# Kernel optimization log

Hardware: AMD Instinct MI355X
Metric: run time of the kernel (lower is better)

The kernel has to match this reference:

```python
import jax, jax.numpy as jnp
import numpy as np

N_STATE = 128      # HiPPO state size (hardcoded N=128 in module)
SEQ = 8192         # sequence length
D_HEAD = 16        # d_model=128 // n_head=8, used only for score scaling
OUT_DIM = 1000     # hardcoded self.out_dim
STEP = 1e-3        # step_size


def _legs_matrices(N):
    # HiPPO-LegS: A[n,k] = -sqrt(2n+1)sqrt(2k+1) (n>k), -(n+1) (n==k), 0 else; B[n]=sqrt(2n+1)
    n = np.arange(N, dtype=np.float64)
    pre = np.sqrt(2.0 * n + 1.0)
    A = -np.tril(pre[:, None] * pre[None, :], -1) - np.diag(n + 1.0)
    B = pre.copy()
    return A, B


def setup_inputs() -> dict:
    key = jax.random.key(0)
    kq, kk, kv, kw = jax.random.split(key, 4)
    A_np, B_np = _legs_matrices(N_STATE)
    A = jnp.asarray(A_np, jnp.float32)
    B = jnp.asarray(B_np, jnp.float32)
    # ZOH discretization (GBT_alpha=2.0 > 1 in repo => zero-order hold)
    GA = jax.scipy.linalg.expm(STEP * A)                       # (N, N)
    GB = jnp.linalg.solve(A, (GA - jnp.eye(N_STATE)) @ B)      # (N,)
    # xavier-uniform proj kernel (128 -> 1000), zero bias
    lim = float(np.sqrt(6.0 / (N_STATE + OUT_DIM)))
    Wp = jax.random.uniform(kw, (N_STATE, OUT_DIM), jnp.float32, -lim, lim)
    bp = jnp.zeros((OUT_DIM,), jnp.float32)
    return {
        "query": jax.random.normal(kq, (SEQ, 1), jnp.float32),
        "key": jax.random.normal(kk, (SEQ, 1), jnp.float32),
        "value": jax.random.normal(kv, (SEQ, 1), jnp.float32),
        "GA": GA,
        "GB": GB,
        "Wp": Wp,
        "bp": bp,
    }


def _hippo_scan(GA, GB, fs):
    # fs: (3, S) scalar input sequences; carry c: (3, N)
    def step(c, ft):
        c = c @ GA.T + ft[:, None] * GB[None, :]
        return c, c
    c0 = jnp.zeros((fs.shape[0], GA.shape[0]), GA.dtype)
    _, cs = jax.lax.scan(step, c0, fs.T)   # cs: (S, 3, N)
    return cs


def reference(query, key, value, GA, GB, Wp, bp):
    fs = jnp.stack([query[:, 0], key[:, 0], value[:, 0]])  # (3, S)
    cs = _hippo_scan(GA, GB, fs)                            # (S, 3, N)
    q, k, v = cs[:, 0, :], cs[:, 1, :], cs[:, 2, :]         # (S, N) each
    score = (q @ k.T) / jnp.sqrt(jnp.asarray(D_HEAD, q.dtype))  # (S, S)
    attn = jax.nn.softmax(score, axis=-1)
    context = attn @ v                                      # (S, N)
    out = context @ Wp + bp                                 # (S, OUT_DIM)
    return out, attn
```

## Files before the change

kernel.cpp:

```cpp
#include <hip/hip_runtime.h>

static constexpr int N  = 128;
static constexpr int S  = 8192;
static constexpr int L  = 128;
static constexpr int NC = 64;
static constexpr int OD = 1000;
static constexpr int KSPLIT = 16;
#define SCL 0.25f

typedef unsigned short u16;
typedef __attribute__((ext_vector_type(4))) unsigned short us4;
typedef __attribute__((ext_vector_type(8))) unsigned short us8;
typedef __attribute__((ext_vector_type(8))) short bf16x8;
typedef __attribute__((ext_vector_type(4))) float f32x4;

__device__ __forceinline__ u16 f2bf(float x){
  unsigned u = __float_as_uint(x);
  u += 0x7FFFu + ((u >> 16) & 1u);
  return (u16)(u >> 16);
}
__device__ __forceinline__ float bf2f(u16 h){
  return __uint_as_float(((unsigned)h) << 16);
}

__global__ void k_copyT(const float* __restrict__ GA, float* __restrict__ QT1){
  int idx = blockIdx.x*256 + threadIdx.x;
  int m = idx >> 7, n = idx & 127;
  QT1[idx] = GA[n*N + m];
}

__global__ __launch_bounds__(256) void k_powmm(float* QT, int mlev){
  int i = blockIdx.z + 1;
  const float* Am = QT + (size_t)mlev*(N*N);
  const float* Ai = QT + (size_t)i*(N*N);
  float* C = QT + (size_t)(mlev+i)*(N*N);
  __shared__ __align__(16) float As[16][68];
  __shared__ __align__(16) float Bs[16][68];
  int bm = blockIdx.y, bn = blockIdx.x;
  int tx = threadIdx.x, ty = threadIdx.y;
  int tid = ty*16 + tx;
  float acc[4][4] = {};
  for (int kt = 0; kt < N; kt += 16){
    int row = tid >> 2, kc = (tid & 3) << 2;
    float4 av = *(const float4*)(Am + (size_t)(bm*64+row)*N + kt + kc);
    As[kc+0][row]=av.x; As[kc+1][row]=av.y; As[kc+2][row]=av.z; As[kc+3][row]=av.w;
    int bk = tid >> 4, c0 = (tid & 15) << 2;
    *(float4*)&Bs[bk][c0] = *(const float4*)(Ai + (size_t)(kt+bk)*N + bn*64 + c0);
    __syncthreads();
#pragma unroll
    for (int kk = 0; kk < 16; ++kk){
      float4 a = *(const float4*)&As[kk][ty*4];
      float4 b = *(const float4*)&Bs[kk][tx*4];
      float aa[4]={a.x,a.y,a.z,a.w}, bb[4]={b.x,b.y,b.z,b.w};
#pragma unroll
      for (int ii=0; ii<4; ++ii)
#pragma unroll
        for (int jj=0; jj<4; ++jj) acc[ii][jj] += aa[ii]*bb[jj];
    }
    __syncthreads();
  }
#pragma unroll
  for (int ii=0; ii<4; ++ii){
    float4 vst = make_float4(acc[ii][0],acc[ii][1],acc[ii][2],acc[ii][3]);
    *(float4*)(C + (size_t)(bm*64+ty*4+ii)*N + bn*64 + tx*4) = vst;
  }
}

__global__ void k_g(const float* __restrict__ QT, const float* __restrict__ GB,
                    float* __restrict__ g){
  int kb = blockIdx.x;
  int n = threadIdx.x;
  if (kb == 0){ g[n] = GB[n]; return; }
  const float* Qk = QT + (size_t)kb*(N*N);
  float acc = 0.0f;
  for (int m = 0; m < N; ++m) acc += Qk[m*N + n]*GB[m];
  g[kb*N + n] = acc;
}

__global__ __launch_bounds__(256) void k_fill_local(const float* __restrict__ fq,
                             const float* __restrict__ fk, const float* __restrict__ fv,
                             const float* __restrict__ g, float* __restrict__ cs){
  int tile = blockIdx.x;
  int s = blockIdx.y, j = blockIdx.z;
  const float* f = (s==0)? fq : (s==1)? fk : fv;
  __shared__ float flp[256];
  __shared__ __align__(16) float Bs[16][68];
  int tx = threadIdx.x, ty = threadIdx.y;
  int tid = ty*16 + tx;
  flp[tid] = (tid < 128) ? 0.0f : f[j*L + tid - 128];
  int ti = tile >> 1, tj = tile & 1;
  float acc[4][4] = {};
  int kmax = (ti == 0) ? 64 : 128;
  for (int kt = 0; kt < kmax; kt += 16){
    int bk = tid >> 4, c0 = (tid & 15) << 2;
    *(float4*)&Bs[bk][c0] = *(const float4*)(g + (size_t)(kt+bk)*N + tj*64 + c0);
    __syncthreads();
#pragma unroll
    for (int kk = 0; kk < 16; ++kk){
      float4 b = *(const float4*)&Bs[kk][tx*4];
      int base = 128 + ti*64 + ty*4 - kt - kk;
      float aa[4] = {flp[base], flp[base+1], flp[base+2], flp[base+3]};
      float bb[4] = {b.x, b.y, b.z, b.w};
#pragma unroll
      for (int ii=0; ii<4; ++ii)
#pragma unroll
        for (int jj=0; jj<4; ++jj) acc[ii][jj] += aa[ii]*bb[jj];
    }
    __syncthreads();
  }
#pragma unroll
  for (int ii=0; ii<4; ++ii){
    int row = ti*64 + ty*4 + ii;
    float4 vst = make_float4(acc[ii][0],acc[ii][1],acc[ii][2],acc[ii][3]);
    *(float4*)(cs + ((size_t)s*S + (size_t)j*L + row)*N + tj*64 + tx*4) = vst;
  }
}

__global__ void k_bscan(const float* __restrict__ QT, const float* __restrict__ cs,
                        float* __restrict__ bounds){
  __shared__ float bc[3][N];
  __shared__ float bnx[3][N];
  int tid = threadIdx.x;
  int s = tid >> 7, n = tid & 127;
  const float* QL = QT + (size_t)L*(N*N);
  bc[s][n] = 0.0f;
  bounds[(0*3+s)*N + n] = 0.0f;
  __syncthreads();
  for (int j = 0; j < NC; ++j){
    float acc = cs[((size_t)s*S + (size_t)j*L + 127)*N + n];
    for (int m = 0; m < N; ++m) acc += QL[m*N+n]*bc[s][m];
    bnx[s][n] = acc;
    bounds[((j+1)*3+s)*N + n] = acc;
    __syncthreads();
    bc[s][n] = bnx[s][n];
    __syncthreads();
  }
}

__global__ __launch_bounds__(256) void k_fill_bound(const float* __restrict__ QT,
                          const float* __restrict__ bounds, float* __restrict__ cs){
  int i = blockIdx.x;
  int jg = blockIdx.y;
  __shared__ float Qs[N*N];
  int tid = threadIdx.x;
  int p = tid >> 7, n = tid & 127;
  const float* Qg = QT + (size_t)(i+1)*(N*N);
  for (int idx = tid; idx < N*N; idx += 256) Qs[idx] = Qg[idx];
  __syncthreads();
  for (int r4 = 0; r4 < 24; r4 += 4){
    int task0 = jg*48 + p*24 + r4;
    const float* b0 = bounds + (size_t)task0*N;
    const float* b1 = b0 + N;
    const float* b2 = b0 + 2*N;
    const float* b3 = b0 + 3*N;
    float a0=0.f, a1=0.f, a2=0.f, a3=0.f;
#pragma unroll 4
    for (int m = 0; m < N; ++m){
      float q = Qs[m*N + n];
      a0 += q*b0[m]; a1 += q*b1[m]; a2 += q*b2[m]; a3 += q*b3[m];
    }
    float av[4] = {a0, a1, a2, a3};
#pragma unroll
    for (int q4 = 0; q4 < 4; ++q4){
      int task = task0 + q4;
      int j = task/3, s2 = task - 3*j;
      cs[((size_t)s2*S + (size_t)j*L + i)*N + n] += av[q4];
    }
  }
}

__global__ void k_split_qk(const float* __restrict__ cs,
                           u16* __restrict__ sh, u16* __restrict__ sl){
  size_t i = ((size_t)blockIdx.x*256 + threadIdx.x) << 2;
  float4 v = *(const float4*)(cs + i);
  us4 h, l;
  h[0]=f2bf(v.x); l[0]=f2bf(v.x - bf2f(h[0]));
  h[1]=f2bf(v.y); l[1]=f2bf(v.y - bf2f(h[1]));
  h[2]=f2bf(v.z); l[2]=f2bf(v.z - bf2f(h[2]));
  h[3]=f2bf(v.w); l[3]=f2bf(v.w - bf2f(h[3]));
  *(us4*)(sh + i) = h;
  *(us4*)(sl + i) = l;
}

__global__ __launch_bounds__(256) void k_split_vT(const float* __restrict__ vs,
                           u16* __restrict__ vth, u16* __restrict__ vtl){
  __shared__ u16 Th[128*72];
  __shared__ u16 Tl[128*72];
  int t0 = blockIdx.x * 64;
  int tid = threadIdx.x;
  for (int c = tid; c < 2048; c += 256){
    int i = c >> 5, n0 = (c & 31) << 2;
    float4 v = *(const float4*)(vs + (size_t)(t0 + i)*N + n0);
    u16 h;
    h = f2bf(v.x); Th[(n0+0)*72 + i] = h; Tl[(n0+0)*72 + i] = f2bf(v.x - bf2f(h));
    h = f2bf(v.y); Th[(n0+1)*72 + i] = h; Tl[(n0+1)*72 + i] = f2bf(v.y - bf2f(h));
    h = f2bf(v.z); Th[(n0+2)*72 + i] = h; Tl[(n0+2)*72 + i] = f2bf(v.z - bf2f(h));
    h = f2bf(v.w); Th[(n0+3)*72 + i] = h; Tl[(n0+3)*72 + i] = f2bf(v.w - bf2f(h));
  }
  __syncthreads();
  for (int c = tid; c < 1024; c += 256){
    int n = c >> 3, tc = (c & 7) << 3;
    *(us8*)(vth + (size_t)n*S + t0 + tc) = *(const us8*)&Th[n*72 + tc];
    *(us8*)(vtl + (size_t)n*S + t0 + tc) = *(const us8*)&Tl[n*72 + tc];
  }
}

__global__ __launch_bounds__(256) void k_score_mfma(
    const u16* __restrict__ qh, const u16* __restrict__ ql,
    const u16* __restrict__ kh, const u16* __restrict__ kl,
    float* __restrict__ attn, float* __restrict__ pmax, float* __restrict__ psum){
  __shared__ __align__(16) u16 smem[4*128*40];
  __shared__ float stats[128][2][2];
  u16* Ah = smem;
  u16* Al = smem + 5120;
  u16* Bh = smem + 10240;
  u16* Bl = smem + 15360;
  int bm = blockIdx.y, bn = blockIdx.x;
  int tid = threadIdx.x;
  int lane = tid & 63, w = tid >> 6;
  int wr = w >> 1, wc = w & 1;
  f32x4 acc[4][4] = {};
  int rA = wr*64 + (lane & 15);
  int rB = wc*64 + (lane & 15);
  int kg = (lane >> 4) << 3;
  for (int kt = 0; kt < N; kt += 32){
    for (int c = tid; c < 512; c += 256){
      int r = c >> 2, k8 = (c & 3) << 3;
      size_t ga = (size_t)(bm*128 + r)*N + kt + k8;
      size_t gb = (size_t)(bn*128 + r)*N + kt + k8;
      int lo = r*40 + k8;
      *(us8*)&Ah[lo] = *(const us8*)(qh + ga);
      *(us8*)&Al[lo] = *(const us8*)(ql + ga);
      *(us8*)&Bh[lo] = *(const us8*)(kh + gb);
      *(us8*)&Bl[lo] = *(const us8*)(kl + gb);
    }
    __syncthreads();
    bf16x8 ah[4], al[4], bh[4], bl[4];
#pragma unroll
    for (int mi = 0; mi < 4; ++mi){
      ah[mi] = *(const bf16x8*)&Ah[(rA + mi*16)*40 + kg];
      al[mi] = *(const bf16x8*)&Al[(rA + mi*16)*40 + kg];
    }
#pragma unroll
    for (int ni = 0; ni < 4; ++ni){
      bh[ni] = *(const bf16x8*)&Bh[(rB + ni*16)*40 + kg];
      bl[ni] = *(const bf16x8*)&Bl[(rB + ni*16)*40 + kg];
    }
#pragma unroll
    for (int mi = 0; mi < 4; ++mi)
#pragma unroll
      for (int ni = 0; ni < 4; ++ni){
        acc[mi][ni] = __builtin_amdgcn_mfma_f32_16x16x32_bf16(ah[mi], bh[ni], acc[mi][ni], 0,0,0);
        acc[mi][ni] = __builtin_amdgcn_mfma_f32_16x16x32_bf16(ah[mi], bl[ni], acc[mi][ni], 0,0,0);
        acc[mi][ni] = __builtin_amdgcn_mfma_f32_16x16x32_bf16(al[mi], bh[ni], acc[mi][ni], 0,0,0);
      }
    __syncthreads();
  }
  float* bounce = (float*)smem;
  int r0l = wr*64 + ((lane >> 4) << 2);
  int c0l = lane & 15;
#pragma unroll
  for (int half = 0; half < 2; ++half){
    if (wc == half){
#pragma unroll
      for (int mi = 0; mi < 4; ++mi)
#pragma unroll
        for (int ni = 0; ni < 4; ++ni)
#pragma unroll
          for (int r = 0; r < 4; ++r)
            bounce[(r0l + mi*16 + r)*68 + ni*16 + c0l] = acc[mi][ni][r]*SCL;
    }
    __syncthreads();
    for (int c = tid; c < 2048; c += 256){
      int r = c >> 4, c4 = (c & 15) << 2;
      *(float4*)(attn + (size_t)(bm*128 + r)*S + bn*128 + half*64 + c4) =
          *(const float4*)&bounce[r*68 + c4];
    }
    if (tid < 128){
      int row = tid;
      float m = -3.0e38f;
      for (int c = 0; c < 64; ++c) m = fmaxf(m, bounce[row*68 + c]);
      float sm = 0.0f;
      for (int c = 0; c < 64; ++c) sm += __expf(bounce[row*68 + c] - m);
      stats[row][half][0] = m; stats[row][half][1] = sm;
    }
    __syncthreads();
  }
  if (tid < 128){
    float m0 = stats[tid][0][0], m1 = stats[tid][1][0];
    float m = fmaxf(m0, m1);
    float Z = stats[tid][0][1]*__expf(m0 - m) + stats[tid][1][1]*__expf(m1 - m);
    pmax[(size_t)bn*S + bm*128 + tid] = m;
    psum[(size_t)bn*S + bm*128 + tid] = Z;
  }
}

__global__ void k_rowstat(const float* __restrict__ pmax, const float* __restrict__ psum,
                          float* __restrict__ rowm, float* __restrict__ rowinv){
  int t = blockIdx.x*256 + threadIdx.x;
  float m = -3.0e38f;
  for (int b = 0; b < 64; ++b) m = fmaxf(m, pmax[(size_t)b*S + t]);
  float Z = 0.0f;
  for (int b = 0; b < 64; ++b) Z += psum[(size_t)b*S + t]*__expf(pmax[(size_t)b*S + t] - m);
  rowm[t] = m;
  rowinv[t] = 1.0f/Z;
}

__global__ __launch_bounds__(256) void k_context_mfma(float* __restrict__ attn,
                       const float* __restrict__ rowm, const float* __restrict__ rowinv,
                       const u16* __restrict__ vth, const u16* __restrict__ vtl,
                       float* __restrict__ dst, int mode){
  __shared__ u16 Ah[128*40], Al[128*40], Bh[128*40], Bl[128*40];
  __shared__ float rm[128], ri[128];
  int kz = blockIdx.x, bm = blockIdx.y;
  int tid = threadIdx.x;
  int lane = tid & 63, w = tid >> 6;
  int wr = w >> 1, wc = w & 1;
  const int KC = S / KSPLIT;
  int k0 = kz*KC;
  if (tid < 128){ rm[tid] = rowm[bm*128 + tid]; ri[tid] = rowinv[bm*128 + tid]; }
  __syncthreads();
  f32x4 acc[4][4] = {};
  int rA = wr*64 + (lane & 15);
  int rB = wc*64 + (lane & 15);
  int kg = (lane >> 4) << 3;
  for (int kt = 0; kt < KC; kt += 32){
    for (int c = tid; c < 1024; c += 256){
      int r = c >> 3, c4 = (c & 7) << 2;
      size_t gaddr = (size_t)(bm*128 + r)*S + k0 + kt + c4;
      float4 v = *(const float4*)(attn + gaddr);
      float m = rm[r], z = ri[r];
      v.x = __expf(v.x - m)*z; v.y = __expf(v.y - m)*z;
      v.z = __expf(v.z - m)*z; v.w = __expf(v.w - m)*z;
      *(float4*)(attn + gaddr) = v;
      us4 h, l;
      h[0]=f2bf(v.x); l[0]=f2bf(v.x - bf2f(h[0]));
      h[1]=f2bf(v.y); l[1]=f2bf(v.y - bf2f(h[1]));
      h[2]=f2bf(v.z); l[2]=f2bf(v.z - bf2f(h[2]));
      h[3]=f2bf(v.w); l[3]=f2bf(v.w - bf2f(h[3]));
      int lo = r*40 + c4;
      *(us4*)&Ah[lo] = h;
      *(us4*)&Al[lo] = l;
    }
    for (int c = tid; c < 512; c += 256){
      int n = c >> 2, k8 = (c & 3) << 3;
      size_t gb = (size_t)n*S + k0 + kt + k8;
      int lo = n*40 + k8;
      *(us8*)&Bh[lo] = *(const us8*)(vth + gb);
      *(us8*)&Bl[lo] = *(const us8*)(vtl + gb);
    }
    __syncthreads();
    bf16x8 ah[4], al[4], bh[4], bl[4];
#pragma unroll
    for (int mi = 0; mi < 4; ++mi){
      ah[mi] = *(const bf16x8*)&Ah[(rA + mi*16)*40 + kg];
      al[mi] = *(const bf16x8*)&Al[(rA + mi*16)*40 + kg];
    }
#pragma unroll
    for (int ni = 0; ni < 4; ++ni){
      bh[ni] = *(const bf16x8*)&Bh[(rB + ni*16)*40 + kg];
      bl[ni] = *(const bf16x8*)&Bl[(rB + ni*16)*40 + kg];
    }
#pragma unroll
    for (int mi = 0; mi < 4; ++mi)
#pragma unroll
      for (int ni = 0; ni < 4; ++ni){
        acc[mi][ni] = __builtin_amdgcn_mfma_f32_16x16x32_bf16(ah[mi], bh[ni], acc[mi][ni], 0,0,0);
        acc[mi][ni] = __builtin_amdgcn_mfma_f32_16x16x32_bf16(ah[mi], bl[ni], acc[mi][ni], 0,0,0);
        acc[mi][ni] = __builtin_amdgcn_mfma_f32_16x16x32_bf16(al[mi], bh[ni], acc[mi][ni], 0,0,0);
      }
    __syncthreads();
  }
  int r0 = bm*128 + wr*64 + ((lane >> 4) << 2);
  int c0 = wc*64 + (lane & 15);
  if (mode == 0){
    float* P = dst + (size_t)kz*S*N;
#pragma unroll
    for (int mi = 0; mi < 4; ++mi)
#pragma unroll
      for (int ni = 0; ni < 4; ++ni)
#pragma unroll
        for (int r = 0; r < 4; ++r)
          P[(size_t)(r0 + mi*16 + r)*N + c0 + ni*16] = acc[mi][ni][r];
  } else {
#pragma unroll
    for (int mi = 0; mi < 4; ++mi)
#pragma unroll
      for (int ni = 0; ni < 4; ++ni)
#pragma unroll
        for (int r = 0; r < 4; ++r)
          atomicAdd(&dst[(size_t)(r0 + mi*16 + r)*N + c0 + ni*16], acc[mi][ni][r]);
  }
}

__global__ __launch_bounds__(256) void k_reduce(const float* __restrict__ part,
                                                float* __restrict__ ctx){
  size_t idx = (size_t)blockIdx.x*256 + threadIdx.x;
  const float4* p4 = (const float4*)part;
  float4 acc = p4[idx];
  const size_t stride = (size_t)S*N/4;
#pragma unroll
  for (int kz = 1; kz < KSPLIT; ++kz){
    float4 v = p4[(size_t)kz*stride + idx];
    acc.x += v.x; acc.y += v.y; acc.z += v.z; acc.w += v.w;
  }
  ((float4*)ctx)[idx] = acc;
}

__global__ __launch_bounds__(256) void k_out(const float* __restrict__ ctx,
                   const float* __restrict__ Wp, const float* __restrict__ bp,
                   float* __restrict__ out){
  __shared__ __align__(16) float As[16][68];
  __shared__ __align__(16) float Bs[16][68];
  int bn = blockIdx.x;
  int bm = blockIdx.y;
  int tx = threadIdx.x, ty = threadIdx.y;
  int tid = ty*16 + tx;
  float acc[4][4] = {};
  for (int kt = 0; kt < N; kt += 16){
    int row = tid >> 2, kc = (tid & 3) << 2;
    float4 av = *(const float4*)(ctx + (size_t)(bm*64+row)*N + kt + kc);
    As[kc+0][row]=av.x; As[kc+1][row]=av.y; As[kc+2][row]=av.z; As[kc+3][row]=av.w;
    int bk = tid >> 4, c0 = (tid & 15) << 2;
#pragma unroll
    for (int jj = 0; jj < 4; ++jj){
      int c = bn*64 + c0 + jj;
      Bs[bk][c0+jj] = (c < OD) ? Wp[(size_t)(kt+bk)*OD + c] : 0.0f;
    }
    __syncthreads();
#pragma unroll
    for (int kk = 0; kk < 16; ++kk){
      float4 a = *(const float4*)&As[kk][ty*4];
      float4 b = *(const float4*)&Bs[kk][tx*4];
      float aa[4]={a.x,a.y,a.z,a.w}, bb[4]={b.x,b.y,b.z,b.w};
#pragma unroll
      for (int ii=0; ii<4; ++ii)
#pragma unroll
        for (int jj=0; jj<4; ++jj) acc[ii][jj] += aa[ii]*bb[jj];
    }
    __syncthreads();
  }
#pragma unroll
  for (int ii=0; ii<4; ++ii){
    int r = bm*64 + ty*4 + ii;
#pragma unroll
    for (int jj=0; jj<4; ++jj){
      int c = bn*64 + tx*4 + jj;
      if (c < OD) out[(size_t)r*OD + c] = acc[ii][jj] + bp[c];
    }
  }
}

extern "C" void kernel_launch(void* const* d_in, const int* in_sizes, int n_in,
                              void* d_out, int out_size, void* d_ws, size_t ws_size,
                              hipStream_t stream){
  const float* fq = (const float*)d_in[0];
  const float* fk = (const float*)d_in[1];
  const float* fv = (const float*)d_in[2];
  const float* GA = (const float*)d_in[3];
  const float* GB = (const float*)d_in[4];
  const float* Wp = (const float*)d_in[5];
  const float* bp = (const float*)d_in[6];
  float* out  = (float*)d_out;
  float* attn = out + (size_t)S*OD;

  float* ws     = (float*)d_ws;
  float* QT     = ws;
  float* g      = QT + (size_t)129*N*N;
  float* bounds = g + (size_t)L*N;
  float* cs     = bounds + (size_t)(NC+1)*3*N;
  float* ctx    = cs + (size_t)3*S*N;
  u16*   qkh    = (u16*)(ctx + (size_t)S*N);
  u16*   qkl    = qkh + (size_t)2*S*N;
  u16*   vth    = qkl + (size_t)2*S*N;
  u16*   vtl    = vth + (size_t)S*N;
  float* pmax   = (float*)(vtl + (size_t)S*N);
  float* psum   = pmax + (size_t)(S/128)*S;
  float* rowm   = psum + (size_t)(S/128)*S;
  float* rowinv = rowm + S;
  float* part   = rowinv + S;
  size_t need_part = ((size_t)(part - ws) + (size_t)KSPLIT*S*N) * sizeof(float);
  bool use_part = (ws_size >= need_part);

  k_copyT<<<64, 256, 0, stream>>>(GA, QT + (size_t)N*N);
  for (int m = 1; m < L; m <<= 1)
    k_powmm<<<dim3(2,2,m), dim3(16,16), 0, stream>>>(QT, m);
  k_g<<<128, 128, 0, stream>>>(QT, GB, g);
  k_fill_local<<<dim3(4,3,NC), dim3(16,16), 0, stream>>>(fq, fk, fv, g, cs);
  k_bscan<<<1, 384, 0, stream>>>(QT, cs, bounds);
  k_fill_bound<<<dim3(L,4), 256, 0, stream>>>(QT, bounds, cs);

  k_split_qk<<<(2*S*N)/1024, 256, 0, stream>>>(cs, qkh, qkl);
  k_split_vT<<<S/64, 256, 0, stream>>>(cs + (size_t)2*S*N, vth, vtl);

  k_score_mfma<<<dim3(S/128, S/128), 256, 0, stream>>>(
      qkh, qkl, qkh + (size_t)S*N, qkl + (size_t)S*N, attn, pmax, psum);
  k_rowstat<<<S/256, 256, 0, stream>>>(pmax, psum, rowm, rowinv);
  if (use_part){
    k_context_mfma<<<dim3(KSPLIT, S/128), 256, 0, stream>>>(attn, rowm, rowinv, vth, vtl, part, 0);
    k_reduce<<<(S*N/4)/256, 256, 0, stream>>>(part, ctx);
  } else {
    hipMemsetAsync(ctx, 0, (size_t)S*N*sizeof(float), stream);
    k_context_mfma<<<dim3(KSPLIT, S/128), 256, 0, stream>>>(attn, rowm, rowinv, vth, vtl, ctx, 1);
  }
  k_out<<<dim3(16, S/64), dim3(16,16), 0, stream>>>(ctx, Wp, bp, out);
}
```

Before: 892.7 us.

## Load MFMA operands directly from global and widen context K tile

The score kernel drops LDS staging of the Q/K bf16 hi/lo tiles and reads MFMA fragments straight from global memory. It also writes the full 128-column tile to a single bounce buffer, so row stats are computed in one pass instead of two halves. The context kernel stops staging V in LDS, loading V fragments directly from global, and processes a 64-wide K chunk per barrier. KSPLIT is halved from 16 to 8. These changes cut LDS traffic and barriers, at the cost of redundant, less coalesced global loads and fewer context blocks running in parallel.

Result: slower. 980.8 us (+9.9%).

```diff
diff --git a/kernel.cpp b/kernel.cpp
--- a/kernel.cpp
+++ b/kernel.cpp
@@ -5,7 +5,7 @@
 static constexpr int L  = 128;
 static constexpr int NC = 64;
 static constexpr int OD = 1000;
-static constexpr int KSPLIT = 16;
+static constexpr int KSPLIT = 8;
 #define SCL 0.25f
 
 typedef unsigned short u16;
@@ -209,42 +209,24 @@
     const u16* __restrict__ qh, const u16* __restrict__ ql,
     const u16* __restrict__ kh, const u16* __restrict__ kl,
     float* __restrict__ attn, float* __restrict__ pmax, float* __restrict__ psum){
-  __shared__ __align__(16) u16 smem[4*128*40];
-  __shared__ float stats[128][2][2];
-  u16* Ah = smem;
-  u16* Al = smem + 5120;
-  u16* Bh = smem + 10240;
-  u16* Bl = smem + 15360;
+  __shared__ __align__(16) float bounce[128*132];
   int bm = blockIdx.y, bn = blockIdx.x;
   int tid = threadIdx.x;
   int lane = tid & 63, w = tid >> 6;
   int wr = w >> 1, wc = w & 1;
   f32x4 acc[4][4] = {};
-  int rA = wr*64 + (lane & 15);
-  int rB = wc*64 + (lane & 15);
+  int rA = bm*128 + wr*64 + (lane & 15);
+  int rB = bn*128 + wc*64 + (lane & 15);
   int kg = (lane >> 4) << 3;
   for (int kt = 0; kt < N; kt += 32){
-    for (int c = tid; c < 512; c += 256){
-      int r = c >> 2, k8 = (c & 3) << 3;
-      size_t ga = (size_t)(bm*128 + r)*N + kt + k8;
-      size_t gb = (size_t)(bn*128 + r)*N + kt + k8;
-      int lo = r*40 + k8;
-      *(us8*)&Ah[lo] = *(const us8*)(qh + ga);
-      *(us8*)&Al[lo] = *(const us8*)(ql + ga);
-      *(us8*)&Bh[lo] = *(const us8*)(kh + gb);
-      *(us8*)&Bl[lo] = *(const us8*)(kl + gb);
-    }
-    __syncthreads();
+    int k = kt + kg;
     bf16x8 ah[4], al[4], bh[4], bl[4];
 #pragma unroll
-    for (int mi = 0; mi < 4; ++mi){
-      ah[mi] = *(const bf16x8*)&Ah[(rA + mi*16)*40 + kg];
-      al[mi] = *(const bf16x8*)&Al[(rA + mi*16)*40 + kg];
-    }
-#pragma unroll
-    for (int ni = 0; ni < 4; ++ni){
-      bh[ni] = *(const bf16x8*)&Bh[(rB + ni*16)*40 + kg];
-      bl[ni] = *(const bf16x8*)&Bl[(rB + ni*16)*40 + kg];
+    for (int i = 0; i < 4; ++i){
+      ah[i] = *(const bf16x8*)(qh + (size_t)(rA + i*16)*N + k);
+      al[i] = *(const bf16x8*)(ql + (size_t)(rA + i*16)*N + k);
+      bh[i] = *(const bf16x8*)(kh + (size_t)(rB + i*16)*N + k);
+      bl[i] = *(const bf16x8*)(kl + (size_t)(rB + i*16)*N + k);
     }
 #pragma unroll
     for (int mi = 0; mi < 4; ++mi)
@@ -254,44 +236,36 @@
         acc[mi][ni] = __builtin_amdgcn_mfma_f32_16x16x32_bf16(ah[mi], bl[ni], acc[mi][ni], 0,0,0);
         acc[mi][ni] = __builtin_amdgcn_mfma_f32_16x16x32_bf16(al[mi], bh[ni], acc[mi][ni], 0,0,0);
       }
-    __syncthreads();
-  }
-  float* bounce = (float*)smem;
+  }
   int r0l = wr*64 + ((lane >> 4) << 2);
-  int c0l = lane & 15;
-#pragma unroll
-  for (int half = 0; half < 2; ++half){
-    if (wc == half){
-#pragma unroll
-      for (int mi = 0; mi < 4; ++mi)
-#pragma unroll
-        for (int ni = 0; ni < 4; ++ni)
-#pragma unroll
-          for (int r = 0; r < 4; ++r)
-            bounce[(r0l + mi*16 + r)*68 + ni*16 + c0l] = acc[mi][ni][r]*SCL;
-    }
-    __syncthreads();
-    for (int c = tid; c < 2048; c += 256){
-      int r = c >> 4, c4 = (c & 15) << 2;
-      *(float4*)(attn + (size_t)(bm*128 + r)*S + bn*128 + half*64 + c4) =
-          *(const float4*)&bounce[r*68 + c4];
-    }
-    if (tid < 128){
-      int row = tid;
-      float m = -3.0e38f;
-      for (int c = 0; c < 64; ++c) m = fmaxf(m, bounce[row*68 + c]);
-      float sm = 0.0f;
-      for (int c = 0; c < 64; ++c) sm += __expf(bounce[row*68 + c] - m);
-      stats[row][half][0] = m; stats[row][half][1] = sm;
-    }
-    __syncthreads();
+  int c0l = wc*64 + (lane & 15);
+#pragma unroll
+  for (int mi = 0; mi < 4; ++mi)
+#pragma unroll
+    for (int ni = 0; ni < 4; ++ni)
+#pragma unroll
+      for (int r = 0; r < 4; ++r)
+        bounce[(r0l + mi*16 + r)*132 + c0l + ni*16] = acc[mi][ni][r]*SCL;
+  __syncthreads();
+  for (int c = tid; c < 4096; c += 256){
+    int r = c >> 5, c4 = (c & 31) << 2;
+    *(float4*)(attn + (size_t)(bm*128 + r)*S + bn*128 + c4) =
+        *(const float4*)&bounce[r*132 + c4];
   }
   if (tid < 128){
-    float m0 = stats[tid][0][0], m1 = stats[tid][1][0];
-    float m = fmaxf(m0, m1);
-    float Z = stats[tid][0][1]*__expf(m0 - m) + stats[tid][1][1]*__expf(m1 - m);
+    const float* row = &bounce[tid*132];
+    float m = -3.0e38f;
+    for (int c4 = 0; c4 < 128; c4 += 4){
+      float4 v = *(const float4*)&row[c4];
+      m = fmaxf(m, fmaxf(fmaxf(v.x,v.y), fmaxf(v.z,v.w)));
+    }
+    float sm = 0.0f;
+    for (int c4 = 0; c4 < 128; c4 += 4){
+      float4 v = *(const float4*)&row[c4];
+      sm += __expf(v.x-m) + __expf(v.y-m) + __expf(v.z-m) + __expf(v.w-m);
+    }
     pmax[(size_t)bn*S + bm*128 + tid] = m;
-    psum[(size_t)bn*S + bm*128 + tid] = Z;
+    psum[(size_t)bn*S + bm*128 + tid] = sm;
   }
 }
 
@@ -310,7 +284,7 @@
                        const float* __restrict__ rowm, const float* __restrict__ rowinv,
                        const u16* __restrict__ vth, const u16* __restrict__ vtl,
                        float* __restrict__ dst, int mode){
-  __shared__ u16 Ah[128*40], Al[128*40], Bh[128*40], Bl[128*40];
+  __shared__ __align__(16) u16 Ah[128*72], Al[128*72];
   __shared__ float rm[128], ri[128];
   int kz = blockIdx.x, bm = blockIdx.y;
   int tid = threadIdx.x;
@@ -322,12 +296,12 @@
   __syncthreads();
   f32x4 acc[4][4] = {};
   int rA = wr*64 + (lane & 15);
-  int rB = wc*64 + (lane & 15);
+  int nB = wc*64 + (lane & 15);
   int kg = (lane >> 4) << 3;
-  for (int kt = 0; kt < KC; kt += 32){
-    for (int c = tid; c < 1024; c += 256){
-      int r = c >> 3, c4 = (c & 7) << 2;
-      size_t gaddr = (size_t)(bm*128 + r)*S + k0 + kt + c4;
+  for (int ko = 0; ko < KC; ko += 64){
+    for (int c = tid; c < 2048; c += 256){
+      int r = c >> 4, c4 = (c & 15) << 2;
+      size_t gaddr = (size_t)(bm*128 + r)*S + k0 + ko + c4;
       float4 v = *(const float4*)(attn + gaddr);
       float m = rm[r], z = ri[r];
       v.x = __expf(v.x - m)*z; v.y = __expf(v.y - m)*z;
@@ -338,37 +312,33 @@
       h[1]=f2bf(v.y); l[1]=f2bf(v.y - bf2f(h[1]));
       h[2]=f2bf(v.z); l[2]=f2bf(v.z - bf2f(h[2]));
       h[3]=f2bf(v.w); l[3]=f2bf(v.w - bf2f(h[3]));
-      int lo = r*40 + c4;
+      int lo = r*72 + c4;
       *(us4*)&Ah[lo] = h;
       *(us4*)&Al[lo] = l;
     }
-    for (int c = tid; c < 512; c += 256){
-      int n = c >> 2, k8 = (c & 3) << 3;
-      size_t gb = (size_t)n*S + k0 + kt + k8;
-      int lo = n*40 + k8;
-      *(us8*)&Bh[lo] = *(const us8*)(vth + gb);
-      *(us8*)&Bl[lo] = *(const us8*)(vtl + gb);
-    }
-    __syncthreads();
-    bf16x8 ah[4], al[4], bh[4], bl[4];
-#pragma unroll
-    for (int mi = 0; mi < 4; ++mi){
-      ah[mi] = *(const bf16x8*)&Ah[(rA + mi*16)*40 + kg];
-      al[mi] = *(const bf16x8*)&Al[(rA + mi*16)*40 + kg];
-    }
-#pragma unroll
-    for (int ni = 0; ni < 4; ++ni){
-      bh[ni] = *(const bf16x8*)&Bh[(rB + ni*16)*40 + kg];
-      bl[ni] = *(const bf16x8*)&Bl[(rB + ni*16)*40 + kg];
-    }
-#pragma unroll
-    for (int mi = 0; mi < 4; ++mi)
+    __syncthreads();
+#pragma unroll
+    for (int k2 = 0; k2 < 2; ++k2){
+      int kk = k2*32 + kg;
+      bf16x8 ah[4], al[4];
+#pragma unroll
+      for (int mi = 0; mi < 4; ++mi){
+        ah[mi] = *(const bf16x8*)&Ah[(rA + mi*16)*72 + kk];
+        al[mi] = *(const bf16x8*)&Al[(rA + mi*16)*72 + kk];
+      }
 #pragma unroll
       for (int ni = 0; ni < 4; ++ni){
-        acc[mi][ni] = __builtin_amdgcn_mfma_f32_16x16x32_bf16(ah[mi], bh[ni], acc[mi][ni], 0,0,0);
-        acc[mi][ni] = __builtin_amdgcn_mfma_f32_16x16x32_bf16(ah[mi], bl[ni], acc[mi][ni], 0,0,0);
-        acc[mi][ni] = __builtin_amdgcn_mfma_f32_16x16x32_bf16(al[mi], bh[ni], acc[mi][ni], 0,0,0);
+        size_t gb = (size_t)(nB + ni*16)*S + k0 + ko + kk;
+        bf16x8 bh = *(const bf16x8*)(vth + gb);
+        bf16x8 bl = *(const bf16x8*)(vtl + gb);
+#pragma unroll
+        for (int mi = 0; mi < 4; ++mi){
+          acc[mi][ni] = __builtin_amdgcn_mfma_f32_16x16x32_bf16(ah[mi], bh, acc[mi][ni], 0,0,0);
+          acc[mi][ni] = __builtin_amdgcn_mfma_f32_16x16x32_bf16(ah[mi], bl, acc[mi][ni], 0,0,0);
+          acc[mi][ni] = __builtin_amdgcn_mfma_f32_16x16x32_bf16(al[mi], bh, acc[mi][ni], 0,0,0);
+        }
       }
+    }
     __syncthreads();
   }
   int r0 = bm*128 + wr*64 + ((lane >> 4) << 2);
```

## Fuse score recomputation with softmax and context GEMM, stats-only first pass

Applied to the files above, without the earlier changes.

The score kernel now only computes per-row softmax max/sum in registers with wave shuffles, and no longer writes raw scores to the attention matrix. The context kernel recomputes QK^T per 32-key chunk from resident Q fragments, applies the normalized softmax, writes attn once, and feeds the probabilities straight into the PV MFMAs. V^T is stored in a tiled layout so each chunk loads contiguously. This removes one full write and one read of the 8192x8192 fp32 attention matrix in exchange for computing QK^T twice and running half-empty MFMA operands (K=16 padded to 32) in the PV step.

Result: no change. 896.8 us (+0.5%).

```diff
diff --git a/kernel.cpp b/kernel.cpp
--- a/kernel.cpp
+++ b/kernel.cpp
@@ -200,29 +200,27 @@
   __syncthreads();
   for (int c = tid; c < 1024; c += 256){
     int n = c >> 3, tc = (c & 7) << 3;
-    *(us8*)(vth + (size_t)n*S + t0 + tc) = *(const us8*)&Th[n*72 + tc];
-    *(us8*)(vtl + (size_t)n*S + t0 + tc) = *(const us8*)&Tl[n*72 + tc];
-  }
-}
-
-__global__ __launch_bounds__(256) void k_score_mfma(
+    int tile = (t0 + tc) >> 5;
+    int kin  = (t0 + tc) & 31;
+    size_t dst = (size_t)tile*4096 + n*32 + kin;
+    *(us8*)(vth + dst) = *(const us8*)&Th[n*72 + tc];
+    *(us8*)(vtl + dst) = *(const us8*)&Tl[n*72 + tc];
+  }
+}
+
+__global__ __launch_bounds__(256) void k_stats(
     const u16* __restrict__ qh, const u16* __restrict__ ql,
     const u16* __restrict__ kh, const u16* __restrict__ kl,
-    float* __restrict__ attn, float* __restrict__ pmax, float* __restrict__ psum){
-  __shared__ __align__(16) u16 smem[4*128*40];
-  __shared__ float stats[128][2][2];
-  u16* Ah = smem;
-  u16* Al = smem + 5120;
-  u16* Bh = smem + 10240;
-  u16* Bl = smem + 15360;
+    float* __restrict__ pmax, float* __restrict__ psum){
+  __shared__ __align__(16) u16 Ah[128*40], Al[128*40], Bh[128*40], Bl[128*40];
+  __shared__ float wst[2][128][2];
   int bm = blockIdx.y, bn = blockIdx.x;
   int tid = threadIdx.x;
   int lane = tid & 63, w = tid >> 6;
+  int l15 = lane & 15, l4 = lane >> 4;
   int wr = w >> 1, wc = w & 1;
-  f32x4 acc[4][4] = {};
-  int rA = wr*64 + (lane & 15);
-  int rB = wc*64 + (lane & 15);
-  int kg = (lane >> 4) << 3;
+  int kg = l4 << 3;
+  f32x4 accs[4][4] = {};
   for (int kt = 0; kt < N; kt += 32){
     for (int c = tid; c < 512; c += 256){
       int r = c >> 2, k8 = (c & 3) << 3;
@@ -235,61 +233,69 @@
       *(us8*)&Bl[lo] = *(const us8*)(kl + gb);
     }
     __syncthreads();
-    bf16x8 ah[4], al[4], bh[4], bl[4];
-#pragma unroll
-    for (int mi = 0; mi < 4; ++mi){
-      ah[mi] = *(const bf16x8*)&Ah[(rA + mi*16)*40 + kg];
-      al[mi] = *(const bf16x8*)&Al[(rA + mi*16)*40 + kg];
-    }
-#pragma unroll
-    for (int ni = 0; ni < 4; ++ni){
-      bh[ni] = *(const bf16x8*)&Bh[(rB + ni*16)*40 + kg];
-      bl[ni] = *(const bf16x8*)&Bl[(rB + ni*16)*40 + kg];
-    }
-#pragma unroll
-    for (int mi = 0; mi < 4; ++mi)
-#pragma unroll
-      for (int ni = 0; ni < 4; ++ni){
-        acc[mi][ni] = __builtin_amdgcn_mfma_f32_16x16x32_bf16(ah[mi], bh[ni], acc[mi][ni], 0,0,0);
-        acc[mi][ni] = __builtin_amdgcn_mfma_f32_16x16x32_bf16(ah[mi], bl[ni], acc[mi][ni], 0,0,0);
-        acc[mi][ni] = __builtin_amdgcn_mfma_f32_16x16x32_bf16(al[mi], bh[ni], acc[mi][ni], 0,0,0);
+    bf16x8 kfh[4], kfl[4], qfh[4], qfl[4];
+#pragma unroll
+    for (int si = 0; si < 4; ++si){
+      kfh[si] = *(const bf16x8*)&Bh[(wr*64 + si*16 + l15)*40 + kg];
+      kfl[si] = *(const bf16x8*)&Bl[(wr*64 + si*16 + l15)*40 + kg];
+    }
+#pragma unroll
+    for (int qi = 0; qi < 4; ++qi){
+      qfh[qi] = *(const bf16x8*)&Ah[(wc*64 + qi*16 + l15)*40 + kg];
+      qfl[qi] = *(const bf16x8*)&Al[(wc*64 + qi*16 + l15)*40 + kg];
+    }
+#pragma unroll
+    for (int si = 0; si < 4; ++si)
+#pragma unroll
+      for (int qi = 0; qi < 4; ++qi){
+        accs[si][qi] = __builtin_amdgcn_mfma_f32_16x16x32_bf16(kfh[si], qfh[qi], accs[si][qi], 0,0,0);
+        accs[si][qi] = __builtin_amdgcn_mfma_f32_16x16x32_bf16(kfh[si], qfl[qi], accs[si][qi], 0,0,0);
+        accs[si][qi] = __builtin_amdgcn_mfma_f32_16x16x32_bf16(kfl[si], qfh[qi], accs[si][qi], 0,0,0);
       }
     __syncthreads();
   }
-  float* bounce = (float*)smem;
-  int r0l = wr*64 + ((lane >> 4) << 2);
-  int c0l = lane & 15;
-#pragma unroll
-  for (int half = 0; half < 2; ++half){
-    if (wc == half){
-#pragma unroll
-      for (int mi = 0; mi < 4; ++mi)
-#pragma unroll
-        for (int ni = 0; ni < 4; ++ni)
-#pragma unroll
-          for (int r = 0; r < 4; ++r)
-            bounce[(r0l + mi*16 + r)*68 + ni*16 + c0l] = acc[mi][ni][r]*SCL;
-    }
-    __syncthreads();
-    for (int c = tid; c < 2048; c += 256){
-      int r = c >> 4, c4 = (c & 15) << 2;
-      *(float4*)(attn + (size_t)(bm*128 + r)*S + bn*128 + half*64 + c4) =
-          *(const float4*)&bounce[r*68 + c4];
-    }
-    if (tid < 128){
-      int row = tid;
-      float m = -3.0e38f;
-      for (int c = 0; c < 64; ++c) m = fmaxf(m, bounce[row*68 + c]);
-      float sm = 0.0f;
-      for (int c = 0; c < 64; ++c) sm += __expf(bounce[row*68 + c] - m);
-      stats[row][half][0] = m; stats[row][half][1] = sm;
-    }
-    __syncthreads();
-  }
+  float mq[4], sq[4];
+#pragma unroll
+  for (int qi = 0; qi < 4; ++qi){
+    float m = -3.0e38f;
+#pragma unroll
+    for (int si = 0; si < 4; ++si)
+#pragma unroll
+      for (int r = 0; r < 4; ++r) m = fmaxf(m, accs[si][qi][r]);
+    mq[qi] = m * SCL;
+  }
+#pragma unroll
+  for (int qi = 0; qi < 4; ++qi){
+    mq[qi] = fmaxf(mq[qi], __shfl_xor(mq[qi], 16, 64));
+    mq[qi] = fmaxf(mq[qi], __shfl_xor(mq[qi], 32, 64));
+  }
+#pragma unroll
+  for (int qi = 0; qi < 4; ++qi){
+    float s = 0.0f;
+#pragma unroll
+    for (int si = 0; si < 4; ++si)
+#pragma unroll
+      for (int r = 0; r < 4; ++r) s += __expf(accs[si][qi][r]*SCL - mq[qi]);
+    sq[qi] = s;
+  }
+#pragma unroll
+  for (int qi = 0; qi < 4; ++qi){
+    sq[qi] += __shfl_xor(sq[qi], 16, 64);
+    sq[qi] += __shfl_xor(sq[qi], 32, 64);
+  }
+  if (l4 == 0){
+#pragma unroll
+    for (int qi = 0; qi < 4; ++qi){
+      int ql_ = wc*64 + qi*16 + l15;
+      wst[wr][ql_][0] = mq[qi];
+      wst[wr][ql_][1] = sq[qi];
+    }
+  }
+  __syncthreads();
   if (tid < 128){
-    float m0 = stats[tid][0][0], m1 = stats[tid][1][0];
+    float m0 = wst[0][tid][0], m1 = wst[1][tid][0];
     float m = fmaxf(m0, m1);
-    float Z = stats[tid][0][1]*__expf(m0 - m) + stats[tid][1][1]*__expf(m1 - m);
+    float Z = wst[0][tid][1]*__expf(m0 - m) + wst[1][tid][1]*__expf(m1 - m);
     pmax[(size_t)bn*S + bm*128 + tid] = m;
     psum[(size_t)bn*S + bm*128 + tid] = Z;
   }
@@ -306,90 +312,132 @@
   rowinv[t] = 1.0f/Z;
 }
 
-__global__ __launch_bounds__(256) void k_context_mfma(float* __restrict__ attn,
-                       const float* __restrict__ rowm, const float* __restrict__ rowinv,
-                       const u16* __restrict__ vth, const u16* __restrict__ vtl,
-                       float* __restrict__ dst, int mode){
-  __shared__ u16 Ah[128*40], Al[128*40], Bh[128*40], Bl[128*40];
-  __shared__ float rm[128], ri[128];
-  int kz = blockIdx.x, bm = blockIdx.y;
-  int tid = threadIdx.x;
-  int lane = tid & 63, w = tid >> 6;
-  int wr = w >> 1, wc = w & 1;
+__global__ __launch_bounds__(256) void k_ctx(
+    float* __restrict__ attn,
+    const float* __restrict__ rowm, const float* __restrict__ rowinv,
+    const u16* __restrict__ qh, const u16* __restrict__ ql,
+    const u16* __restrict__ kh, const u16* __restrict__ kl,
+    const u16* __restrict__ vth, const u16* __restrict__ vtl,
+    float* __restrict__ dst, int mode){
+  __shared__ __align__(16) u16 Ksh[32*136], Ksl[32*136];
+  __shared__ __align__(16) u16 Vsh[128*40], Vsl[128*40];
+  int bm = blockIdx.x, kz = blockIdx.y;
+  int tid = threadIdx.x, lane = tid & 63, w = tid >> 6;
+  int l15 = lane & 15, l4 = lane >> 4;
+  int kg = l4 << 3;
   const int KC = S / KSPLIT;
   int k0 = kz*KC;
-  if (tid < 128){ rm[tid] = rowm[bm*128 + tid]; ri[tid] = rowinv[bm*128 + tid]; }
-  __syncthreads();
-  f32x4 acc[4][4] = {};
-  int rA = wr*64 + (lane & 15);
-  int rB = wc*64 + (lane & 15);
-  int kg = (lane >> 4) << 3;
-  for (int kt = 0; kt < KC; kt += 32){
-    for (int c = tid; c < 1024; c += 256){
-      int r = c >> 3, c4 = (c & 7) << 2;
-      size_t gaddr = (size_t)(bm*128 + r)*S + k0 + kt + c4;
-      float4 v = *(const float4*)(attn + gaddr);
-      float m = rm[r], z = ri[r];
-      v.x = __expf(v.x - m)*z; v.y = __expf(v.y - m)*z;
-      v.z = __expf(v.z - m)*z; v.w = __expf(v.w - m)*z;
-      *(float4*)(attn + gaddr) = v;
-      us4 h, l;
-      h[0]=f2bf(v.x); l[0]=f2bf(v.x - bf2f(h[0]));
-      h[1]=f2bf(v.y); l[1]=f2bf(v.y - bf2f(h[1]));
-      h[2]=f2bf(v.z); l[2]=f2bf(v.z - bf2f(h[2]));
-      h[3]=f2bf(v.w); l[3]=f2bf(v.w - bf2f(h[3]));
-      int lo = r*40 + c4;
-      *(us4*)&Ah[lo] = h;
-      *(us4*)&Al[lo] = l;
-    }
+  int qrow0 = bm*128 + w*32;
+  bf16x8 qfh[2][4], qfl[2][4];
+  float rm[2], ri[2];
+#pragma unroll
+  for (int qi = 0; qi < 2; ++qi){
+    int q = qrow0 + qi*16 + l15;
+#pragma unroll
+    for (int kt = 0; kt < 4; ++kt){
+      qfh[qi][kt] = *(const bf16x8*)(qh + (size_t)q*N + kt*32 + kg);
+      qfl[qi][kt] = *(const bf16x8*)(ql + (size_t)q*N + kt*32 + kg);
+    }
+    rm[qi] = rowm[q];
+    ri[qi] = rowinv[q];
+  }
+  f32x4 acco[2][8] = {};
+  for (int ko = 0; ko < KC/32; ++ko){
+    int cb = k0 + ko*32;
     for (int c = tid; c < 512; c += 256){
-      int n = c >> 2, k8 = (c & 3) << 3;
-      size_t gb = (size_t)n*S + k0 + kt + k8;
-      int lo = n*40 + k8;
-      *(us8*)&Bh[lo] = *(const us8*)(vth + gb);
-      *(us8*)&Bl[lo] = *(const us8*)(vtl + gb);
-    }
-    __syncthreads();
-    bf16x8 ah[4], al[4], bh[4], bl[4];
-#pragma unroll
-    for (int mi = 0; mi < 4; ++mi){
-      ah[mi] = *(const bf16x8*)&Ah[(rA + mi*16)*40 + kg];
-      al[mi] = *(const bf16x8*)&Al[(rA + mi*16)*40 + kg];
-    }
-#pragma unroll
-    for (int ni = 0; ni < 4; ++ni){
-      bh[ni] = *(const bf16x8*)&Bh[(rB + ni*16)*40 + kg];
-      bl[ni] = *(const bf16x8*)&Bl[(rB + ni*16)*40 + kg];
-    }
-#pragma unroll
-    for (int mi = 0; mi < 4; ++mi)
-#pragma unroll
-      for (int ni = 0; ni < 4; ++ni){
-        acc[mi][ni] = __builtin_amdgcn_mfma_f32_16x16x32_bf16(ah[mi], bh[ni], acc[mi][ni], 0,0,0);
-        acc[mi][ni] = __builtin_amdgcn_mfma_f32_16x16x32_bf16(ah[mi], bl[ni], acc[mi][ni], 0,0,0);
-        acc[mi][ni] = __builtin_amdgcn_mfma_f32_16x16x32_bf16(al[mi], bh[ni], acc[mi][ni], 0,0,0);
+      int rr = c >> 4, k8 = (c & 15) << 3;
+      size_t gk = (size_t)(cb + rr)*N + k8;
+      *(us8*)&Ksh[rr*136 + k8] = *(const us8*)(kh + gk);
+      *(us8*)&Ksl[rr*136 + k8] = *(const us8*)(kl + gk);
+    }
+    {
+      const u16* sh = vth + (size_t)(cb >> 5)*4096;
+      const u16* sl = vtl + (size_t)(cb >> 5)*4096;
+      for (int c = tid; c < 512; c += 256){
+        int n = c >> 2, k8 = (c & 3) << 3;
+        *(us8*)&Vsh[n*40 + k8] = *(const us8*)(sh + (size_t)c*8);
+        *(us8*)&Vsl[n*40 + k8] = *(const us8*)(sl + (size_t)c*8);
       }
-    __syncthreads();
-  }
-  int r0 = bm*128 + wr*64 + ((lane >> 4) << 2);
-  int c0 = wc*64 + (lane & 15);
+    }
+    __syncthreads();
+    f32x4 accs[2][2] = {};
+#pragma unroll
+    for (int kt = 0; kt < 4; ++kt){
+      bf16x8 kfh[2], kfl[2];
+#pragma unroll
+      for (int si = 0; si < 2; ++si){
+        kfh[si] = *(const bf16x8*)&Ksh[(si*16 + l15)*136 + kt*32 + kg];
+        kfl[si] = *(const bf16x8*)&Ksl[(si*16 + l15)*136 + kt*32 + kg];
+      }
+#pragma unroll
+      for (int si = 0; si < 2; ++si)
+#pragma unroll
+        for (int qi = 0; qi < 2; ++qi){
+          accs[si][qi] = __builtin_amdgcn_mfma_f32_16x16x32_bf16(kfh[si], qfh[qi][kt], accs[si][qi], 0,0,0);
+          accs[si][qi] = __builtin_amdgcn_mfma_f32_16x16x32_bf16(kfh[si], qfl[qi][kt], accs[si][qi], 0,0,0);
+          accs[si][qi] = __builtin_amdgcn_mfma_f32_16x16x32_bf16(kfl[si], qfh[qi][kt], accs[si][qi], 0,0,0);
+        }
+    }
+    bf16x8 pah[2][2], pal[2][2];
+#pragma unroll
+    for (int si = 0; si < 2; ++si)
+#pragma unroll
+      for (int qi = 0; qi < 2; ++qi){
+        float p0 = __expf(accs[si][qi][0]*SCL - rm[qi]) * ri[qi];
+        float p1 = __expf(accs[si][qi][1]*SCL - rm[qi]) * ri[qi];
+        float p2 = __expf(accs[si][qi][2]*SCL - rm[qi]) * ri[qi];
+        float p3 = __expf(accs[si][qi][3]*SCL - rm[qi]) * ri[qi];
+        int q = qrow0 + qi*16 + l15;
+        *(float4*)(attn + (size_t)q*S + cb + si*16 + (l4<<2)) = make_float4(p0,p1,p2,p3);
+        u16 h0=f2bf(p0), h1=f2bf(p1), h2=f2bf(p2), h3=f2bf(p3);
+        u16 e0=f2bf(p0-bf2f(h0)), e1=f2bf(p1-bf2f(h1)), e2=f2bf(p2-bf2f(h2)), e3=f2bf(p3-bf2f(h3));
+        bf16x8 ah; ah[0]=(short)h0; ah[1]=(short)h1; ah[2]=(short)h2; ah[3]=(short)h3;
+        ah[4]=0; ah[5]=0; ah[6]=0; ah[7]=0;
+        bf16x8 al; al[0]=(short)e0; al[1]=(short)e1; al[2]=(short)e2; al[3]=(short)e3;
+        al[4]=0; al[5]=0; al[6]=0; al[7]=0;
+        pah[si][qi] = ah; pal[si][qi] = al;
+      }
+#pragma unroll
+    for (int si = 0; si < 2; ++si)
+#pragma unroll
+      for (int ni = 0; ni < 8; ++ni){
+        int vaddr = (ni*16 + l15)*40 + si*16 + (l4<<2);
+        us4 vh4 = *(const us4*)&Vsh[vaddr];
+        us4 vl4 = *(const us4*)&Vsl[vaddr];
+        bf16x8 vh; vh[0]=(short)vh4[0]; vh[1]=(short)vh4[1]; vh[2]=(short)vh4[2]; vh[3]=(short)vh4[3];
+        vh[4]=0; vh[5]=0; vh[6]=0; vh[7]=0;
+        bf16x8 vl; vl[0]=(short)vl4[0]; vl[1]=(short)vl4[1]; vl[2]=(short)vl4[2]; vl[3]=(short)vl4[3];
+        vl[4]=0; vl[5]=0; vl[6]=0; vl[7]=0;
+#pragma unroll
+        for (int qi = 0; qi < 2; ++qi){
+          acco[qi][ni] = __builtin_amdgcn_mfma_f32_16x16x32_bf16(pah[si][qi], vh, acco[qi][ni], 0,0,0);
+          acco[qi][ni] = __builtin_amdgcn_mfma_f32_16x16x32_bf16(pah[si][qi], vl, acco[qi][ni], 0,0,0);
+          acco[qi][ni] = __builtin_amdgcn_mfma_f32_16x16x32_bf16(pal[si][qi], vh, acco[qi][ni], 0,0,0);
+        }
+      }
+    __syncthreads();
+  }
   if (mode == 0){
     float* P = dst + (size_t)kz*S*N;
 #pragma unroll
-    for (int mi = 0; mi < 4; ++mi)
-#pragma unroll
-      for (int ni = 0; ni < 4; ++ni)
-#pragma unroll
-        for (int r = 0; r < 4; ++r)
-          P[(size_t)(r0 + mi*16 + r)*N + c0 + ni*16] = acc[mi][ni][r];
+    for (int qi = 0; qi < 2; ++qi)
+#pragma unroll
+      for (int ni = 0; ni < 8; ++ni)
+#pragma unroll
+        for (int r = 0; r < 4; ++r){
+          int q = qrow0 + qi*16 + (l4<<2) + r;
+          P[(size_t)q*N + ni*16 + l15] = acco[qi][ni][r];
+        }
   } else {
 #pragma unroll
-    for (int mi = 0; mi < 4; ++mi)
-#pragma unroll
-      for (int ni = 0; ni < 4; ++ni)
-#pragma unroll
-        for (int r = 0; r < 4; ++r)
-          atomicAdd(&dst[(size_t)(r0 + mi*16 + r)*N + c0 + ni*16], acc[mi][ni][r]);
+    for (int qi = 0; qi < 2; ++qi)
+#pragma unroll
+      for (int ni = 0; ni < 8; ++ni)
+#pragma unroll
+        for (int r = 0; r < 4; ++r){
+          int q = qrow0 + qi*16 + (l4<<2) + r;
+          atomicAdd(&dst[(size_t)q*N + ni*16 + l15], acco[qi][ni][r]);
+        }
   }
 }
 
@@ -493,15 +541,17 @@
   k_split_qk<<<(2*S*N)/1024, 256, 0, stream>>>(cs, qkh, qkl);
   k_split_vT<<<S/64, 256, 0, stream>>>(cs + (size_t)2*S*N, vth, vtl);
 
-  k_score_mfma<<<dim3(S/128, S/128), 256, 0, stream>>>(
-      qkh, qkl, qkh + (size_t)S*N, qkl + (size_t)S*N, attn, pmax, psum);
+  k_stats<<<dim3(S/128, S/128), 256, 0, stream>>>(
+      qkh, qkl, qkh + (size_t)S*N, qkl + (size_t)S*N, pmax, psum);
   k_rowstat<<<S/256, 256, 0, stream>>>(pmax, psum, rowm, rowinv);
   if (use_part){
-    k_context_mfma<<<dim3(KSPLIT, S/128), 256, 0, stream>>>(attn, rowm, rowinv, vth, vtl, part, 0);
+    k_ctx<<<dim3(S/128, KSPLIT), 256, 0, stream>>>(attn, rowm, rowinv,
+        qkh, qkl, qkh + (size_t)S*N, qkl + (size_t)S*N, vth, vtl, part, 0);
     k_reduce<<<(S*N/4)/256, 256, 0, stream>>>(part, ctx);
   } else {
     hipMemsetAsync(ctx, 0, (size_t)S*N*sizeof(float), stream);
-    k_context_mfma<<<dim3(KSPLIT, S/128), 256, 0, stream>>>(attn, rowm, rowinv, vth, vtl, ctx, 1);
+    k_ctx<<<dim3(S/128, KSPLIT), 256, 0, stream>>>(attn, rowm, rowinv,
+        qkh, qkl, qkh + (size_t)S*N, qkl + (size_t)S*N, vth, vtl, ctx, 1);
   }
   k_out<<<dim3(16, S/64), dim3(16,16), 0, stream>>>(ctx, Wp, bp, out);
 }
```
